# Kernel optimization log

Measured on AMD Instinct MI355X. Metric: run time of the kernel, lower is better.

## Reference

```python
import jax, jax.numpy as jnp
import numpy as np

N = 500_000        # nodes
F = 128            # node feature dim
E = 4_000_000      # edges
B = 4              # graphs in batch
COORD_RANGE = 256.0
VOXEL = 8.0        # voxel_size (same per dim, from init size=[8,8,8])
G = int(COORD_RANGE // VOXEL)   # 32 voxels per dim
V = B * G * G * G               # fixed number of voxel slots
EFFECTIVE_RADIUS = 8.0          # Cartesian max_value


def setup_inputs() -> dict:
    key = jax.random.key(0)
    k1, k2, k3 = jax.random.split(key, 3)
    x = jax.random.normal(k1, (N, F), dtype=jnp.float32)
    pos = jax.random.uniform(k2, (N, 3), dtype=jnp.float32) * COORD_RANGE
    # sorted segment ids: B contiguous graphs
    batch = ((jnp.arange(N) * B) // N).astype(jnp.int32)
    edge_index = jax.random.randint(k3, (2, E), 0, N, dtype=jnp.int64)
    return {"x": x, "pos": pos, "batch": batch, "edge_index": edge_index}


def reference(x, pos, batch, edge_index):
    # ---- voxel_grid: assign each node to a (batch, voxel) cluster ----
    v = jnp.clip(jnp.floor(pos / VOXEL).astype(jnp.int32), 0, G - 1)  # [N,3]
    vid = batch * (G * G * G) + v[:, 0] * (G * G) + v[:, 1] * G + v[:, 2]  # [N]

    # ---- max_pool: scatter-max features, mean positions per cluster ----
    pooled_x = jax.ops.segment_max(x, vid, num_segments=V)            # [V,F]
    count = jax.ops.segment_sum(jnp.ones((N,), x.dtype), vid, num_segments=V)  # [V]
    occupied = count > 0
    pooled_x = jnp.where(occupied[:, None], pooled_x, 0.0)
    pooled_pos = jax.ops.segment_sum(pos, vid, num_segments=V) / jnp.maximum(count, 1.0)[:, None]  # [V,3]

    # ---- remap edges to clusters; mask self-loops (coalesce approximated by mask) ----
    src = vid[edge_index[0]]  # [E]
    dst = vid[edge_index[1]]  # [E]
    edge_mask = src != dst
    new_edge_index = jnp.stack([src, dst])  # [2,E]

    # ---- Cartesian(cat=False, norm=True, max_value=effective_radius) ----
    cart = pooled_pos[dst] - pooled_pos[src]                 # [E,3]
    edge_attr = cart / (2.0 * EFFECTIVE_RADIUS) + 0.5
    edge_attr = jnp.where(edge_mask[:, None], edge_attr, 0.0)

    return pooled_x, pooled_pos, new_edge_index, edge_attr, edge_mask
```

## Files before the change

### kernel.cpp

```cpp
#include <hip/hip_runtime.h>

#define NN 500000
#define FF 128
#define EE 4000000
#define BB 4
#define GG 32
#define VV (BB * GG * GG * GG)

#define OUT_X    0
#define OUT_POS  (VV * FF)
#define OUT_EIDX (OUT_POS + VV * 3)
#define OUT_ATTR (OUT_EIDX + 2 * EE)
#define OUT_MASK (OUT_ATTR + 3 * EE)

__global__ __launch_bounds__(256) void vid_kernel(
    const float* __restrict__ pos, const int* __restrict__ batch,
    int* __restrict__ vid, unsigned int* __restrict__ cnt)
{
    int n = blockIdx.x * 256 + threadIdx.x;
    if (n >= NN) return;
    float px = pos[3 * n + 0], py = pos[3 * n + 1], pz = pos[3 * n + 2];
    int vx = min(max((int)floorf(px * 0.125f), 0), GG - 1);
    int vy = min(max((int)floorf(py * 0.125f), 0), GG - 1);
    int vz = min(max((int)floorf(pz * 0.125f), 0), GG - 1);
    int v = batch[n] * (GG * GG * GG) + vx * (GG * GG) + vy * GG + vz;
    vid[n] = v;
    atomicAdd(&cnt[v], 1u);
}

__global__ __launch_bounds__(256) void scan_local_kernel(
    const unsigned int* __restrict__ cnt, unsigned int* __restrict__ offs,
    unsigned int* __restrict__ bsum)
{
    __shared__ unsigned int s[256];
    int i = blockIdx.x * 256 + threadIdx.x;
    unsigned int val = cnt[i];
    s[threadIdx.x] = val;
    __syncthreads();
    for (int d = 1; d < 256; d <<= 1) {
        unsigned int t = (threadIdx.x >= d) ? s[threadIdx.x - d] : 0u;
        __syncthreads();
        s[threadIdx.x] += t;
        __syncthreads();
    }
    offs[i] = s[threadIdx.x] - val;
    if (threadIdx.x == 255) bsum[blockIdx.x] = s[255];
}

__global__ __launch_bounds__(512) void scan_bsum_kernel(unsigned int* __restrict__ bsum)
{
    __shared__ unsigned int s[512];
    unsigned int val = bsum[threadIdx.x];
    s[threadIdx.x] = val;
    __syncthreads();
    for (int d = 1; d < 512; d <<= 1) {
        unsigned int t = (threadIdx.x >= d) ? s[threadIdx.x - d] : 0u;
        __syncthreads();
        s[threadIdx.x] += t;
        __syncthreads();
    }
    bsum[threadIdx.x] = s[threadIdx.x] - val;
}

__global__ __launch_bounds__(256) void scan_add_kernel(
    unsigned int* __restrict__ offs, const unsigned int* __restrict__ bsum,
    unsigned int* __restrict__ cursor)
{
    int i = blockIdx.x * 256 + threadIdx.x;
    unsigned int o = offs[i] + bsum[blockIdx.x];
    offs[i] = o;
    cursor[i] = o;
}

__global__ __launch_bounds__(256) void scatter_kernel(
    const int* __restrict__ vid, unsigned int* __restrict__ cursor,
    unsigned int* __restrict__ order)
{
    int n = blockIdx.x * 256 + threadIdx.x;
    if (n >= NN) return;
    unsigned int p = atomicAdd(&cursor[vid[n]], 1u);
    order[p] = n;
}

__global__ __launch_bounds__(256) void pool_kernel(
    const float* __restrict__ x, const float* __restrict__ pos,
    const unsigned int* __restrict__ order,
    const unsigned int* __restrict__ offs, const unsigned int* __restrict__ cnt,
    float* __restrict__ out_x, float* __restrict__ out_pos)
{
    int w = threadIdx.x >> 6;
    int lane = threadIdx.x & 63;
    int g = lane >> 4;
    int fl = lane & 15;
    int v = blockIdx.x * 4 + w;
    unsigned int start = offs[v];
    unsigned int c = cnt[v];

    float4 mlo = make_float4(-INFINITY, -INFINITY, -INFINITY, -INFINITY);
    float4 mhi = mlo;
    float sx = 0.0f, sy = 0.0f, sz = 0.0f;

    for (unsigned int base = 0; base < c; base += 64) {
        unsigned int rem = min(c - base, 64u);
        unsigned int idx = (lane < rem) ? order[start + base + lane] : 0u;
        if (lane < rem) {
            const float* pp = pos + 3 * (size_t)idx;
            sx += pp[0]; sy += pp[1]; sz += pp[2];
        }
        for (unsigned int k = (unsigned int)g; k < rem; k += 4) {
            unsigned int n = __shfl(idx, (int)k);
            const float4* row = (const float4*)(x + (size_t)n * FF);
            float4 a = row[fl];
            float4 b = row[fl + 16];
            mlo.x = fmaxf(mlo.x, a.x); mlo.y = fmaxf(mlo.y, a.y);
            mlo.z = fmaxf(mlo.z, a.z); mlo.w = fmaxf(mlo.w, a.w);
            mhi.x = fmaxf(mhi.x, b.x); mhi.y = fmaxf(mhi.y, b.y);
            mhi.z = fmaxf(mhi.z, b.z); mhi.w = fmaxf(mhi.w, b.w);
        }
    }

    #define MERGE(f) f = fmaxf(f, __shfl_xor(f, 16)); f = fmaxf(f, __shfl_xor(f, 32));
    MERGE(mlo.x) MERGE(mlo.y) MERGE(mlo.z) MERGE(mlo.w)
    MERGE(mhi.x) MERGE(mhi.y) MERGE(mhi.z) MERGE(mhi.w)
    #undef MERGE

    float4 res = (lane < 16) ? mlo : mhi;
    if (c == 0) res = make_float4(0.0f, 0.0f, 0.0f, 0.0f);
    if (lane < 32)
        ((float4*)(out_x + (size_t)v * FF))[lane] = res;

    for (int d = 1; d < 64; d <<= 1) {
        sx += __shfl_xor(sx, d);
        sy += __shfl_xor(sy, d);
        sz += __shfl_xor(sz, d);
    }
    if (lane == 0) {
        float inv = 1.0f / fmaxf((float)c, 1.0f);
        out_pos[3 * v + 0] = sx * inv;
        out_pos[3 * v + 1] = sy * inv;
        out_pos[3 * v + 2] = sz * inv;
    }
}

__global__ __launch_bounds__(256) void edge_kernel(
    const int* __restrict__ eidx, const int* __restrict__ vid,
    const float* __restrict__ pooled_pos, float* __restrict__ out)
{
    __shared__ float sattr[768];
    int e0 = blockIdx.x * 256;
    int e = e0 + threadIdx.x;
    int sv = vid[eidx[e]];
    int dv = vid[eidx[EE + e]];
    bool m = (sv != dv);
    out[OUT_EIDX + e] = (float)sv;
    out[OUT_EIDX + EE + e] = (float)dv;
    float ax = 0.0f, ay = 0.0f, az = 0.0f;
    if (m) {
        ax = (pooled_pos[3 * dv + 0] - pooled_pos[3 * sv + 0]) * 0.0625f + 0.5f;
        ay = (pooled_pos[3 * dv + 1] - pooled_pos[3 * sv + 1]) * 0.0625f + 0.5f;
        az = (pooled_pos[3 * dv + 2] - pooled_pos[3 * sv + 2]) * 0.0625f + 0.5f;
    }
    sattr[3 * threadIdx.x + 0] = ax;
    sattr[3 * threadIdx.x + 1] = ay;
    sattr[3 * threadIdx.x + 2] = az;
    out[OUT_MASK + e] = m ? 1.0f : 0.0f;
    __syncthreads();
    float* dst = out + OUT_ATTR + (size_t)3 * e0;
    #pragma unroll
    for (int i = 0; i < 3; ++i)
        dst[i * 256 + threadIdx.x] = sattr[i * 256 + threadIdx.x];
}

extern "C" void kernel_launch(void* const* d_in, const int* in_sizes, int n_in,
                              void* d_out, int out_size, void* d_ws, size_t ws_size,
                              hipStream_t stream)
{
    const float* x     = (const float*)d_in[0];
    const float* pos   = (const float*)d_in[1];
    const int*   batch = (const int*)d_in[2];
    const int*   eidx  = (const int*)d_in[3];
    float* out = (float*)d_out;

    char* ws = (char*)d_ws;
    unsigned int* cnt     = (unsigned int*)(ws + 0);
    int*          vid     = (int*)(ws + 524288);
    unsigned int* offs    = (unsigned int*)(ws + 2524288);
    unsigned int* cursor  = (unsigned int*)(ws + 3048576);
    unsigned int* bsum    = (unsigned int*)(ws + 3572864);
    unsigned int* order   = (unsigned int*)(ws + 3574912);

    hipMemsetAsync(d_ws, 0, 524288, stream);

    vid_kernel<<<(NN + 255) / 256, 256, 0, stream>>>(pos, batch, vid, cnt);
    scan_local_kernel<<<VV / 256, 256, 0, stream>>>(cnt, offs, bsum);
    scan_bsum_kernel<<<1, 512, 0, stream>>>(bsum);
    scan_add_kernel<<<VV / 256, 256, 0, stream>>>(offs, bsum, cursor);
    scatter_kernel<<<(NN + 255) / 256, 256, 0, stream>>>(vid, cursor, order);
    pool_kernel<<<VV / 4, 256, 0, stream>>>(x, pos, order, offs, cnt,
                                            out + OUT_X, out + OUT_POS);
    edge_kernel<<<(EE + 255) / 256, 256, 0, stream>>>(eidx, vid, out + OUT_POS, out);
}
```

Before: 554.4 us.

## Pack voxel meta and padded float4 pooled positions; vectorize edge kernel two per thread

The scan_add kernel now writes a packed (offset,count) uint2 per voxel, so the pool kernel fetches both with one load. The pool kernel also writes each mean position into a 16-byte padded float4 workspace array. The edge kernel then processes two edges per thread with int2/float2 loads and stores, and gathers pooled positions with one float4 load instead of three scalar loads. This cuts memory transactions in the dominant edge pass, at the cost of extra workspace and a few more small writes.

```diff
diff --git a/kernel.cpp b/kernel.cpp
--- a/kernel.cpp
+++ b/kernel.cpp
@@ -63,13 +63,14 @@
 }
 
 __global__ __launch_bounds__(256) void scan_add_kernel(
-    unsigned int* __restrict__ offs, const unsigned int* __restrict__ bsum,
-    unsigned int* __restrict__ cursor)
+    const unsigned int* __restrict__ offs_in, const unsigned int* __restrict__ bsum,
+    const unsigned int* __restrict__ cnt,
+    unsigned int* __restrict__ cursor, uint2* __restrict__ meta)
 {
     int i = blockIdx.x * 256 + threadIdx.x;
-    unsigned int o = offs[i] + bsum[blockIdx.x];
-    offs[i] = o;
+    unsigned int o = offs_in[i] + bsum[blockIdx.x];
     cursor[i] = o;
+    meta[i] = make_uint2(o, cnt[i]);
 }
 
 __global__ __launch_bounds__(256) void scatter_kernel(
@@ -84,17 +85,18 @@
 
 __global__ __launch_bounds__(256) void pool_kernel(
     const float* __restrict__ x, const float* __restrict__ pos,
-    const unsigned int* __restrict__ order,
-    const unsigned int* __restrict__ offs, const unsigned int* __restrict__ cnt,
-    float* __restrict__ out_x, float* __restrict__ out_pos)
+    const unsigned int* __restrict__ order, const uint2* __restrict__ meta,
+    float* __restrict__ out_x, float* __restrict__ out_pos,
+    float4* __restrict__ pos4)
 {
     int w = threadIdx.x >> 6;
     int lane = threadIdx.x & 63;
     int g = lane >> 4;
     int fl = lane & 15;
     int v = blockIdx.x * 4 + w;
-    unsigned int start = offs[v];
-    unsigned int c = cnt[v];
+    uint2 mt = meta[v];
+    unsigned int start = mt.x;
+    unsigned int c = mt.y;
 
     float4 mlo = make_float4(-INFINITY, -INFINITY, -INFINITY, -INFINITY);
     float4 mhi = mlo;
@@ -136,39 +138,57 @@
     }
     if (lane == 0) {
         float inv = 1.0f / fmaxf((float)c, 1.0f);
-        out_pos[3 * v + 0] = sx * inv;
-        out_pos[3 * v + 1] = sy * inv;
-        out_pos[3 * v + 2] = sz * inv;
+        float mx = sx * inv, my = sy * inv, mz = sz * inv;
+        out_pos[3 * v + 0] = mx;
+        out_pos[3 * v + 1] = my;
+        out_pos[3 * v + 2] = mz;
+        pos4[v] = make_float4(mx, my, mz, 0.0f);
     }
 }
 
 __global__ __launch_bounds__(256) void edge_kernel(
     const int* __restrict__ eidx, const int* __restrict__ vid,
-    const float* __restrict__ pooled_pos, float* __restrict__ out)
-{
-    __shared__ float sattr[768];
-    int e0 = blockIdx.x * 256;
-    int e = e0 + threadIdx.x;
-    int sv = vid[eidx[e]];
-    int dv = vid[eidx[EE + e]];
-    bool m = (sv != dv);
-    out[OUT_EIDX + e] = (float)sv;
-    out[OUT_EIDX + EE + e] = (float)dv;
-    float ax = 0.0f, ay = 0.0f, az = 0.0f;
-    if (m) {
-        ax = (pooled_pos[3 * dv + 0] - pooled_pos[3 * sv + 0]) * 0.0625f + 0.5f;
-        ay = (pooled_pos[3 * dv + 1] - pooled_pos[3 * sv + 1]) * 0.0625f + 0.5f;
-        az = (pooled_pos[3 * dv + 2] - pooled_pos[3 * sv + 2]) * 0.0625f + 0.5f;
-    }
-    sattr[3 * threadIdx.x + 0] = ax;
-    sattr[3 * threadIdx.x + 1] = ay;
-    sattr[3 * threadIdx.x + 2] = az;
-    out[OUT_MASK + e] = m ? 1.0f : 0.0f;
+    const float4* __restrict__ pos4, float* __restrict__ out)
+{
+    __shared__ float sattr[1536];
+    int t = threadIdx.x;
+    size_t e0 = (size_t)blockIdx.x * 512;
+    int rem = (int)((EE - e0 < 512) ? (EE - e0) : 512);
+    size_t p = e0 / 2 + t;
+    float a0x = 0.f, a0y = 0.f, a0z = 0.f, a1x = 0.f, a1y = 0.f, a1z = 0.f;
+    if (2 * t < rem) {
+        int2 s2 = ((const int2*)eidx)[p];
+        int2 d2 = ((const int2*)(eidx + EE))[p];
+        int sv0 = vid[s2.x], sv1 = vid[s2.y];
+        int dv0 = vid[d2.x], dv1 = vid[d2.y];
+        bool m0 = (sv0 != dv0), m1 = (sv1 != dv1);
+        ((float2*)(out + OUT_EIDX))[p]      = make_float2((float)sv0, (float)sv1);
+        ((float2*)(out + OUT_EIDX + EE))[p] = make_float2((float)dv0, (float)dv1);
+        ((float2*)(out + OUT_MASK))[p]      = make_float2(m0 ? 1.f : 0.f, m1 ? 1.f : 0.f);
+        if (m0) {
+            float4 ps = pos4[sv0], pd = pos4[dv0];
+            a0x = (pd.x - ps.x) * 0.0625f + 0.5f;
+            a0y = (pd.y - ps.y) * 0.0625f + 0.5f;
+            a0z = (pd.z - ps.z) * 0.0625f + 0.5f;
+        }
+        if (m1) {
+            float4 ps = pos4[sv1], pd = pos4[dv1];
+            a1x = (pd.x - ps.x) * 0.0625f + 0.5f;
+            a1y = (pd.y - ps.y) * 0.0625f + 0.5f;
+            a1z = (pd.z - ps.z) * 0.0625f + 0.5f;
+        }
+    }
+    sattr[6 * t + 0] = a0x; sattr[6 * t + 1] = a0y; sattr[6 * t + 2] = a0z;
+    sattr[6 * t + 3] = a1x; sattr[6 * t + 4] = a1y; sattr[6 * t + 5] = a1z;
     __syncthreads();
-    float* dst = out + OUT_ATTR + (size_t)3 * e0;
+    float2* dst = (float2*)(out + OUT_ATTR + 3 * e0);
+    const float2* sp = (const float2*)sattr;
+    int nf2 = 3 * rem / 2;
     #pragma unroll
-    for (int i = 0; i < 3; ++i)
-        dst[i * 256 + threadIdx.x] = sattr[i * 256 + threadIdx.x];
+    for (int i = 0; i < 3; ++i) {
+        int idx = i * 256 + t;
+        if (idx < nf2) dst[idx] = sp[idx];
+    }
 }
 
 extern "C" void kernel_launch(void* const* d_in, const int* in_sizes, int n_in,
@@ -188,15 +208,17 @@
     unsigned int* cursor  = (unsigned int*)(ws + 3048576);
     unsigned int* bsum    = (unsigned int*)(ws + 3572864);
     unsigned int* order   = (unsigned int*)(ws + 3574912);
+    uint2*        meta    = (uint2*)(ws + 5574912);
+    float4*       pos4    = (float4*)(ws + 6623488);
 
     hipMemsetAsync(d_ws, 0, 524288, stream);
 
     vid_kernel<<<(NN + 255) / 256, 256, 0, stream>>>(pos, batch, vid, cnt);
     scan_local_kernel<<<VV / 256, 256, 0, stream>>>(cnt, offs, bsum);
     scan_bsum_kernel<<<1, 512, 0, stream>>>(bsum);
-    scan_add_kernel<<<VV / 256, 256, 0, stream>>>(offs, bsum, cursor);
+    scan_add_kernel<<<VV / 256, 256, 0, stream>>>(offs, bsum, cnt, cursor, meta);
     scatter_kernel<<<(NN + 255) / 256, 256, 0, stream>>>(vid, cursor, order);
-    pool_kernel<<<VV / 4, 256, 0, stream>>>(x, pos, order, offs, cnt,
-                                            out + OUT_X, out + OUT_POS);
-    edge_kernel<<<(EE + 255) / 256, 256, 0, stream>>>(eidx, vid, out + OUT_POS, out);
-}
+    pool_kernel<<<VV / 4, 256, 0, stream>>>(x, pos, order, meta,
+                                            out + OUT_X, out + OUT_POS, pos4);
+    edge_kernel<<<(EE + 511) / 512, 256, 0, stream>>>(eidx, vid, pos4, out);
+}
```

After: 557.3 us. About the same (+0.5%).
